# Kernel optimization log

Measured on AMD Instinct MI355X. Metric: run time of the kernel, lower is better.

Reference implementation:

```python
import jax, jax.numpy as jnp
import numpy as np

NUM_EXPERTS = 8
HIDDEN = 2048
FFN = 1376
CAPACITY_FACTOR = 1.25
SCORE_SCALE = 1.0


def setup_inputs() -> dict:
    key = jax.random.key(0)
    k = jax.random.split(key, 6)
    T = 8192
    x = jax.random.normal(k[0], (T, HIDDEN), dtype=jnp.float32)
    topK_indices = jax.random.randint(k[1], (T,), 0, NUM_EXPERTS, dtype=jnp.int64)
    topK_scores = jax.random.uniform(k[2], (T,), dtype=jnp.float32)
    s = 1.0 / np.sqrt(HIDDEN)
    w_gate = jax.random.normal(k[3], (NUM_EXPERTS, HIDDEN, FFN), dtype=jnp.float32) * s
    w_up = jax.random.normal(k[4], (NUM_EXPERTS, HIDDEN, FFN), dtype=jnp.float32) * s
    w_down = jax.random.normal(k[5], (NUM_EXPERTS, FFN, HIDDEN), dtype=jnp.float32) * (1.0 / np.sqrt(FFN))
    return {"x": x, "topK_indices": topK_indices, "topK_scores": topK_scores,
            "w_gate": w_gate, "w_up": w_up, "w_down": w_down}


def reference(x, topK_indices, topK_scores, w_gate, w_up, w_down):
    T, D = x.shape
    E = w_gate.shape[0]
    capacity = int(CAPACITY_FACTOR * T / E)  # static (depends only on shapes)
    # position of each token within its assigned expert (deterministic drop:
    # keep the first `capacity` tokens in sequence order per expert)
    oh = jax.nn.one_hot(topK_indices, E, dtype=jnp.int32)          # [T,E]
    rank = jnp.take_along_axis(jnp.cumsum(oh, axis=0) - 1,
                               topK_indices[:, None].astype(jnp.int32), axis=1)[:, 0]
    keep = rank < capacity                                          # [T]
    # dispatch into per-expert capacity buffers; dropped tokens go to dummy slot
    slot = jnp.where(keep, topK_indices.astype(jnp.int32) * capacity + rank, E * capacity)
    buf = jnp.zeros((E * capacity + 1, D), x.dtype)
    buf = buf.at[slot].set(jnp.where(keep[:, None], x, jnp.zeros_like(x)))
    xe = buf[:E * capacity].reshape(E, capacity, D)                 # [E,C,D]
    # per-expert SwiGLU MLP as grouped GEMMs
    h = jax.nn.silu(jnp.einsum('ecd,edf->ecf', xe, w_gate)) * jnp.einsum('ecd,edf->ecf', xe, w_up)
    out = jnp.einsum('ecf,efd->ecd', h, w_down).reshape(E * capacity, D)
    out = jnp.concatenate([out, jnp.zeros((1, D), out.dtype)], axis=0)
    # combine: dropped tokens -> zero (dropped_padding='zero'), gate-score fusion
    y = out[slot] * keep[:, None].astype(out.dtype)
    y = y * (topK_scores[:, None] * SCORE_SCALE)
    return y
```

## Files before the change

### kernel.cpp

```cpp
#include <hip/hip_runtime.h>
#include <hip/hip_bf16.h>
#include <cstdint>
#include <cstddef>

#define NTOK 8192
#define DH   2048
#define DF   1376
#define DFP  1408
#define NE   8
#define CAP  1280

typedef __bf16 bf16x8 __attribute__((ext_vector_type(8)));
typedef float  f32x4  __attribute__((ext_vector_type(4)));

#define BARRIER() asm volatile("s_barrier" ::: "memory")
#define WAITV(n)  asm volatile("s_waitcnt vmcnt(" #n ")" ::: "memory")
#define SETPRIO(n) __builtin_amdgcn_s_setprio(n)

__device__ __forceinline__ uint32_t pk2(float a, float b) {
  float2 f; f.x = a; f.y = b;
  union { __hip_bfloat162 h; uint32_t u; } cv;
  cv.h = __float22bfloat162_rn(f);
  return cv.u;
}
__device__ __forceinline__ ushort bf16bits(float a) {
  return (ushort)(pk2(a, 0.f) & 0xFFFFu);
}
__device__ __forceinline__ void gload16(const ushort* g, ushort* l) {
  __builtin_amdgcn_global_load_lds(
      (const __attribute__((address_space(1))) uint32_t*)(const void*)g,
      (__attribute__((address_space(3))) uint32_t*)(void*)l,
      16, 0, 0);
}

__device__ __forceinline__ void rp_src(int o, int& row, int& ko) {
  int p = o >> 7;
  int g = ((o >> 4) & 7) ^ (p & 7);
  row = p * 2 + (g >> 2);
  ko  = (g & 3) * 8;
}
__device__ __forceinline__ int rp_off(int row, int l4) {
  return ((row >> 1) << 7) + (((((row & 1) << 2) + l4) ^ ((row >> 1) & 7)) << 4);
}

__global__ void routing_kernel(const int* __restrict__ idx, int* __restrict__ tok_slot,
                               int* __restrict__ tok_keep) {
  __shared__ int cnt[256][NE];
  const int t = threadIdx.x;
  for (int s = t; s < NE * CAP; s += 256) tok_slot[s] = -1;
  unsigned long long cA = 0ull, cB = 0ull;
  const int per = NTOK / 256, base = t * per;
  for (int i = 0; i < per; ++i) {
    int e = idx[base + i];
    unsigned long long inc = 1ull << ((e & 3) * 16);
    if (e < 4) cA += inc; else cB += inc;
  }
#pragma unroll
  for (int e = 0; e < 4; ++e) cnt[t][e]     = (int)((cA >> (e * 16)) & 0xFFFF);
#pragma unroll
  for (int e = 0; e < 4; ++e) cnt[t][4 + e] = (int)((cB >> (e * 16)) & 0xFFFF);
  __syncthreads();
  if (t < NE) {
    int run = 0;
    for (int i = 0; i < 256; ++i) { int c = cnt[i][t]; cnt[i][t] = run; run += c; }
  }
  __syncthreads();
  cA = 0ull; cB = 0ull;
#pragma unroll
  for (int e = 0; e < 4; ++e) cA |= (unsigned long long)(cnt[t][e] & 0xFFFF) << (e * 16);
#pragma unroll
  for (int e = 0; e < 4; ++e) cB |= (unsigned long long)(cnt[t][4 + e] & 0xFFFF) << (e * 16);
  for (int i = 0; i < per; ++i) {
    int token = base + i;
    int e = idx[token];
    int sh = (e & 3) * 16;
    int r = (int)(((e < 4 ? cA : cB) >> sh) & 0xFFFF);
    unsigned long long inc = 1ull << sh;
    if (e < 4) cA += inc; else cB += inc;
    bool keep = (r < CAP);
    tok_keep[token] = keep ? 1 : 0;
    if (keep) tok_slot[e * CAP + r] = token;
  }
}

__global__ void zero_dropped(const int* __restrict__ keep, float* __restrict__ y) {
  if (keep[blockIdx.x]) return;
  float4 z = {0.f, 0.f, 0.f, 0.f};
  float* p = y + (size_t)blockIdx.x * DH + threadIdx.x * 8;
  *(float4*)p = z;
  *(float4*)(p + 4) = z;
}

__global__ void convert_x(const float* __restrict__ x, ushort* __restrict__ xb) {
  int i = (blockIdx.x * 256 + threadIdx.x) * 8;
  float4 a = *(const float4*)(x + i);
  float4 b = *(const float4*)(x + i + 4);
  uint4 p = { pk2(a.x, a.y), pk2(a.z, a.w), pk2(b.x, b.y), pk2(b.z, b.w) };
  *(uint4*)(xb + i) = p;
}

__global__ __launch_bounds__(256) void transpose_cvt(
    const float* __restrict__ in, ushort* __restrict__ out, int K, int N) {
  __shared__ ushort T[64][72];
  const int tid = threadIdx.x;
  const int n0 = blockIdx.x * 64, k0 = blockIdx.y * 64;
  const size_t eoff_in  = (size_t)blockIdx.z * K * N;
  const size_t eoff_out = (size_t)blockIdx.z * N * K;
  const int kr = tid >> 4;
  const int nc = (tid & 15) * 4;
#pragma unroll
  for (int it = 0; it < 4; ++it) {
    int k = k0 + kr + it * 16;
    int n = n0 + nc;
    float4 v = {0.f, 0.f, 0.f, 0.f};
    if (k < K && n + 4 <= N) v = *(const float4*)(in + eoff_in + (size_t)k * N + n);
    T[nc + 0][kr + it * 16] = bf16bits(v.x);
    T[nc + 1][kr + it * 16] = bf16bits(v.y);
    T[nc + 2][kr + it * 16] = bf16bits(v.z);
    T[nc + 3][kr + it * 16] = bf16bits(v.w);
  }
  __syncthreads();
  const int nr = tid >> 2;
  const int kc = tid & 3;
#pragma unroll
  for (int it = 0; it < 2; ++it) {
    int kloc = kc * 16 + it * 8;
    int n = n0 + nr, k = k0 + kloc;
    if (n < N && k + 8 <= K)
      *(uint4*)(out + eoff_out + (size_t)n * K + k) = *(const uint4*)&T[nr][kloc];
  }
}

__global__ void pad_h(ushort* __restrict__ h) {
  int idx = blockIdx.x * 512 + threadIdx.x;
  int row = idx >> 2, q = idx & 3;
  uint4 z = {0u, 0u, 0u, 0u};
  *(uint4*)(h + (size_t)row * DFP + DF + q * 8) = z;
}

__global__ __launch_bounds__(512, 1) void gemm_gateup3(
    const ushort* __restrict__ xb, const ushort* __restrict__ wgt,
    const ushort* __restrict__ wut, const int* __restrict__ tok_slot,
    ushort* __restrict__ h)
{
  __shared__ __align__(16) char sm[131072];
  const int tid = threadIdx.x, lane = tid & 63, wid = tid >> 6;
  const int wr = wid >> 1, wc = wid & 1;
  const int l15 = lane & 15, l4 = lane >> 4;

  int wgid = (blockIdx.x & 7) * 55 + (blockIdx.x >> 3);
  const int e = wgid / 55;
  const int rem = wgid - e * 55;
  const int mt = rem / 11, nt = rem - (rem / 11) * 11;
  const int n0 = nt * 128;

  const ushort* srcA[2]; const ushort* srcBg; const ushort* srcBu;
#pragma unroll
  for (int c = 0; c < 2; ++c) {
    int o = c * 8192 + wid * 1024 + lane * 16;
    int row, ko; rp_src(o, row, ko);
    int tk = tok_slot[e * CAP + mt * 256 + row];
    if (tk < 0) tk = 0;
    srcA[c] = xb + (size_t)tk * DH + ko;
  }
  {
    int o = wid * 1024 + lane * 16;
    int row, ko; rp_src(o, row, ko);
    int n = n0 + row; if (n > DF - 1) n = DF - 1;
    srcBg = wgt + ((size_t)e * DF + n) * DH + ko;
    srcBu = wut + ((size_t)e * DF + n) * DH + ko;
  }
  int aoff[4], boff[4];
#pragma unroll
  for (int i = 0; i < 4; ++i) aoff[i] = rp_off(wr * 64 + i * 16 + l15, l4);
#pragma unroll
  for (int j = 0; j < 4; ++j) boff[j] = rp_off(wc * 64 + j * 16 + l15, l4);
  const int dstw = wid * 1024;

  f32x4 accG[4][4], accU[4][4];
#pragma unroll
  for (int i = 0; i < 4; ++i)
#pragma unroll
    for (int j = 0; j < 4; ++j) {
      accG[i][j] = (f32x4){0.f, 0.f, 0.f, 0.f};
      accU[i][j] = (f32x4){0.f, 0.f, 0.f, 0.f};
    }

  const int NT = DH / 32;
#pragma unroll
  for (int t0 = 0; t0 < 3; ++t0) {
    int kk = t0 * 32;
    gload16(srcA[0] + kk, (ushort*)(sm + t0 * 16384 + dstw));
    gload16(srcA[1] + kk, (ushort*)(sm + t0 * 16384 + 8192 + dstw));
    gload16(srcBg   + kk, (ushort*)(sm + 65536 + t0 * 8192 + dstw));
    gload16(srcBu   + kk, (ushort*)(sm + 98304 + t0 * 8192 + dstw));
  }
  WAITV(8);
  BARRIER();

  for (int t = 0; t < NT; ++t) {
    const int r = t & 3, w = (t + 3) & 3;
    char* Ab  = sm + r * 16384;
    char* Bgb = sm + 65536 + r * 8192;
    char* Bub = sm + 98304 + r * 8192;
    bf16x8 a[4], bg[4], bu[4];
#pragma unroll
    for (int i = 0; i < 4; ++i) a[i]  = *(const bf16x8*)(Ab + aoff[i]);
#pragma unroll
    for (int j = 0; j < 4; ++j) bg[j] = *(const bf16x8*)(Bgb + boff[j]);
#pragma unroll
    for (int j = 0; j < 4; ++j) bu[j] = *(const bf16x8*)(Bub + boff[j]);
    if (t + 3 < NT) {
      int kk = (t + 3) * 32;
      gload16(srcA[0] + kk, (ushort*)(sm + w * 16384 + dstw));
      gload16(srcA[1] + kk, (ushort*)(sm + w * 16384 + 8192 + dstw));
      gload16(srcBg   + kk, (ushort*)(sm + 65536 + w * 8192 + dstw));
      gload16(srcBu   + kk, (ushort*)(sm + 98304 + w * 8192 + dstw));
    }
    SETPRIO(1);
#pragma unroll
    for (int j = 0; j < 4; ++j)
#pragma unroll
      for (int i = 0; i < 4; ++i)
        accG[i][j] = __builtin_amdgcn_mfma_f32_16x16x32_bf16(a[i], bg[j], accG[i][j], 0, 0, 0);
#pragma unroll
    for (int j = 0; j < 4; ++j)
#pragma unroll
      for (int i = 0; i < 4; ++i)
        accU[i][j] = __builtin_amdgcn_mfma_f32_16x16x32_bf16(a[i], bu[j], accU[i][j], 0, 0, 0);
    SETPRIO(0);
    if (t + 3 < NT)      { WAITV(8); }
    else if (t + 2 < NT) { WAITV(4); }
    else if (t + 1 < NT) { WAITV(0); }
    BARRIER();
  }
  const size_t rowbase = (size_t)(e * CAP + mt * 256 + wr * 64);
#pragma unroll
  for (int j = 0; j < 4; ++j) {
    int col = n0 + wc * 64 + j * 16 + l15;
    if (col < DF) {
#pragma unroll
      for (int i = 0; i < 4; ++i)
#pragma unroll
        for (int r2 = 0; r2 < 4; ++r2) {
          size_t row = rowbase + i * 16 + l4 * 4 + r2;
          float gv = accG[i][j][r2], uv = accU[i][j][r2];
          h[row * DFP + col] = bf16bits(gv / (1.f + __expf(-gv)) * uv);
        }
    }
  }
}

__global__ __launch_bounds__(512, 1) void gemm_down3(
    const ushort* __restrict__ h, const ushort* __restrict__ wdt,
    const int* __restrict__ tok_slot, const float* __restrict__ scores,
    float* __restrict__ y)
{
  __shared__ __align__(16) char sm[100352];
  int* tokc = (int*)(sm + 98304);
  float* scc = (float*)(sm + 99328);
  const int tid = threadIdx.x, lane = tid & 63, wid = tid >> 6;
  const int wr = wid >> 1, wc = wid & 1;
  const int l15 = lane & 15, l4 = lane >> 4;

  int wgid = (blockIdx.x & 7) * 80 + (blockIdx.x >> 3);
  const int e = wgid / 80;
  const int rem = wgid - e * 80;
  const int mt = rem / 16, nt = rem & 15;
  const int n0 = nt * 128;

  if (tid < 256) {
    int tk = tok_slot[e * CAP + mt * 256 + tid];
    tokc[tid] = tk;
    scc[tid] = (tk >= 0) ? scores[tk] : 0.f;
  }
  __syncthreads();

  const size_t hrow0 = (size_t)(e * CAP + mt * 256);
  const ushort* srcA[2]; const ushort* srcB;
#pragma unroll
  for (int c = 0; c < 2; ++c) {
    int o = c * 8192 + wid * 1024 + lane * 16;
    int row, ko; rp_src(o, row, ko);
    srcA[c] = h + (hrow0 + row) * DFP + ko;
  }
  {
    int o = wid * 1024 + lane * 16;
    int row, ko; rp_src(o, row, ko);
    srcB = wdt + ((size_t)e * DH + n0 + row) * DF + ko;
  }
  int aoff[4], boff[4];
#pragma unroll
  for (int i = 0; i < 4; ++i) aoff[i] = rp_off(wr * 64 + i * 16 + l15, l4);
#pragma unroll
  for (int j = 0; j < 4; ++j) boff[j] = rp_off(wc * 64 + j * 16 + l15, l4);
  const int dstw = wid * 1024;

  f32x4 acc[4][4];
#pragma unroll
  for (int i = 0; i < 4; ++i)
#pragma unroll
    for (int j = 0; j < 4; ++j) acc[i][j] = (f32x4){0.f, 0.f, 0.f, 0.f};

  const int NT = DFP / 32;
#pragma unroll
  for (int t0 = 0; t0 < 3; ++t0) {
    int kk = t0 * 32;
    gload16(srcA[0] + kk, (ushort*)(sm + t0 * 16384 + dstw));
    gload16(srcA[1] + kk, (ushort*)(sm + t0 * 16384 + 8192 + dstw));
    gload16(srcB    + kk, (ushort*)(sm + 65536 + t0 * 8192 + dstw));
  }
  WAITV(6);
  BARRIER();

  for (int t = 0; t < NT; ++t) {
    const int r = t & 3, w = (t + 3) & 3;
    char* Ab = sm + r * 16384;
    char* Bb = sm + 65536 + r * 8192;
    bf16x8 a[4], b[4];
#pragma unroll
    for (int i = 0; i < 4; ++i) a[i] = *(const bf16x8*)(Ab + aoff[i]);
#pragma unroll
    for (int j = 0; j < 4; ++j) b[j] = *(const bf16x8*)(Bb + boff[j]);
    if (t + 3 < NT) {
      int kk = (t + 3) * 32;
      gload16(srcA[0] + kk, (ushort*)(sm + w * 16384 + dstw));
      gload16(srcA[1] + kk, (ushort*)(sm + w * 16384 + 8192 + dstw));
      gload16(srcB    + kk, (ushort*)(sm + 65536 + w * 8192 + dstw));
    }
    SETPRIO(1);
#pragma unroll
    for (int j = 0; j < 4; ++j)
#pragma unroll
      for (int i = 0; i < 4; ++i)
        acc[i][j] = __builtin_amdgcn_mfma_f32_16x16x32_bf16(a[i], b[j], acc[i][j], 0, 0, 0);
    SETPRIO(0);
    if (t + 3 < NT)      { WAITV(6); }
    else if (t + 2 < NT) { WAITV(3); }
    else if (t + 1 < NT) { WAITV(0); }
    BARRIER();
  }
  int tkr[4][4]; float sr[4][4];
#pragma unroll
  for (int i = 0; i < 4; ++i)
#pragma unroll
    for (int r = 0; r < 4; ++r) {
      int rl = wr * 64 + i * 16 + l4 * 4 + r;
      tkr[i][r] = tokc[rl];
      sr[i][r]  = scc[rl];
    }
#pragma unroll
  for (int j = 0; j < 4; ++j) {
    int col = n0 + wc * 64 + j * 16 + l15;
#pragma unroll
    for (int i = 0; i < 4; ++i)
#pragma unroll
      for (int r = 0; r < 4; ++r)
        if (tkr[i][r] >= 0)
          y[(size_t)tkr[i][r] * DH + col] = acc[i][j][r] * sr[i][r];
  }
}

extern "C" void kernel_launch(void* const* d_in, const int* in_sizes, int n_in,
                              void* d_out, int out_size, void* d_ws, size_t ws_size,
                              hipStream_t stream) {
  const float* x   = (const float*)d_in[0];
  const int*   idx = (const int*)d_in[1];
  const float* sc  = (const float*)d_in[2];
  const float* wg  = (const float*)d_in[3];
  const float* wu  = (const float*)d_in[4];
  const float* wd  = (const float*)d_in[5];
  float* y = (float*)d_out;

  const size_t OFF_KEEP = 40960;
  const size_t OFF_H    = 73728;
  const size_t SZ_H     = (size_t)NE * CAP * DFP * 2;
  const size_t OFF_XB   = OFF_H + SZ_H;
  const size_t SZ_XB    = (size_t)NTOK * DH * 2;
  const size_t OFF_WGT  = OFF_XB + SZ_XB;
  const size_t SZ_W     = (size_t)NE * DH * DF * 2;
  const size_t OFF_WUT  = OFF_WGT + SZ_W;

  int* tok_slot = (int*)d_ws;
  int* tok_keep = (int*)((char*)d_ws + OFF_KEEP);
  ushort* hbuf = (ushort*)((char*)d_ws + OFF_H);
  ushort* xb   = (ushort*)((char*)d_ws + OFF_XB);
  ushort* wgt  = (ushort*)((char*)d_ws + OFF_WGT);
  ushort* wut  = (ushort*)((char*)d_ws + OFF_WUT);
  ushort* wdt  = wgt;

  hipLaunchKernelGGL(routing_kernel, dim3(1), dim3(256), 0, stream, idx, tok_slot, tok_keep);
  hipLaunchKernelGGL(zero_dropped, dim3(NTOK), dim3(256), 0, stream, tok_keep, y);
  hipLaunchKernelGGL(convert_x, dim3(NTOK * DH / 2048), dim3(256), 0, stream, x, xb);
  hipLaunchKernelGGL(transpose_cvt, dim3((DF + 63) / 64, DH / 64, NE), dim3(256), 0, stream,
                     wg, wgt, DH, DF);
  hipLaunchKernelGGL(transpose_cvt, dim3((DF + 63) / 64, DH / 64, NE), dim3(256), 0, stream,
                     wu, wut, DH, DF);
  hipLaunchKernelGGL(pad_h, dim3(80), dim3(512), 0, stream, hbuf);
  hipLaunchKernelGGL(gemm_gateup3, dim3(440), dim3(512), 0, stream,
                     xb, wgt, wut, tok_slot, hbuf);
  hipLaunchKernelGGL(transpose_cvt, dim3(DH / 64, (DF + 63) / 64, NE), dim3(256), 0, stream,
                     wd, wdt, DF, DH);
  hipLaunchKernelGGL(gemm_down3, dim3(640), dim3(512), 0, stream,
                     hbuf, wdt, tok_slot, sc, y);
}
```

Measured before the change: 356.0 us.

## Split GEMM main loops into two barrier-separated phases interleaving loads and MFMAs

Both grouped-GEMM kernels now split each K-step into two halves. Each half issues part of the LDS reads and global-to-LDS prefetches, then runs a barrier, an lgkmcnt wait and a scheduling barrier around half of the MFMA work. The aim is a ping-pong style schedule where memory issue from some waves overlaps matrix math in others, with tighter control over compiler instruction ordering. The cost is extra barriers per iteration, which may add stalls if the waves do not actually stagger.

```diff
diff --git a/kernel.cpp b/kernel.cpp
--- a/kernel.cpp
+++ b/kernel.cpp
@@ -15,6 +15,8 @@
 
 #define BARRIER() asm volatile("s_barrier" ::: "memory")
 #define WAITV(n)  asm volatile("s_waitcnt vmcnt(" #n ")" ::: "memory")
+#define LGKM0()   asm volatile("s_waitcnt lgkmcnt(0)" ::: "memory")
+#define SCHED0()  __builtin_amdgcn_sched_barrier(0)
 #define SETPRIO(n) __builtin_amdgcn_s_setprio(n)
 
 __device__ __forceinline__ uint32_t pk2(float a, float b) {
@@ -203,35 +205,44 @@
     char* Ab  = sm + r * 16384;
     char* Bgb = sm + 65536 + r * 8192;
     char* Bub = sm + 98304 + r * 8192;
+    const int kk = (t + 3) * 32;
     bf16x8 a[4], bg[4], bu[4];
 #pragma unroll
     for (int i = 0; i < 4; ++i) a[i]  = *(const bf16x8*)(Ab + aoff[i]);
 #pragma unroll
     for (int j = 0; j < 4; ++j) bg[j] = *(const bf16x8*)(Bgb + boff[j]);
+    if (t + 3 < NT) {
+      gload16(srcA[0] + kk, (ushort*)(sm + w * 16384 + dstw));
+      gload16(srcA[1] + kk, (ushort*)(sm + w * 16384 + 8192 + dstw));
+    }
+    BARRIER();
+    LGKM0(); SCHED0();
+    SETPRIO(1);
+#pragma unroll
+    for (int j = 0; j < 4; ++j)
+#pragma unroll
+      for (int i = 0; i < 4; ++i)
+        accG[i][j] = __builtin_amdgcn_mfma_f32_16x16x32_bf16(a[i], bg[j], accG[i][j], 0, 0, 0);
+    SETPRIO(0); SCHED0();
+    BARRIER();
 #pragma unroll
     for (int j = 0; j < 4; ++j) bu[j] = *(const bf16x8*)(Bub + boff[j]);
     if (t + 3 < NT) {
-      int kk = (t + 3) * 32;
-      gload16(srcA[0] + kk, (ushort*)(sm + w * 16384 + dstw));
-      gload16(srcA[1] + kk, (ushort*)(sm + w * 16384 + 8192 + dstw));
-      gload16(srcBg   + kk, (ushort*)(sm + 65536 + w * 8192 + dstw));
-      gload16(srcBu   + kk, (ushort*)(sm + 98304 + w * 8192 + dstw));
-    }
-    SETPRIO(1);
-#pragma unroll
-    for (int j = 0; j < 4; ++j)
-#pragma unroll
-      for (int i = 0; i < 4; ++i)
-        accG[i][j] = __builtin_amdgcn_mfma_f32_16x16x32_bf16(a[i], bg[j], accG[i][j], 0, 0, 0);
-#pragma unroll
-    for (int j = 0; j < 4; ++j)
-#pragma unroll
-      for (int i = 0; i < 4; ++i)
-        accU[i][j] = __builtin_amdgcn_mfma_f32_16x16x32_bf16(a[i], bu[j], accU[i][j], 0, 0, 0);
-    SETPRIO(0);
+      gload16(srcBg + kk, (ushort*)(sm + 65536 + w * 8192 + dstw));
+      gload16(srcBu + kk, (ushort*)(sm + 98304 + w * 8192 + dstw));
+    }
     if (t + 3 < NT)      { WAITV(8); }
     else if (t + 2 < NT) { WAITV(4); }
     else if (t + 1 < NT) { WAITV(0); }
+    BARRIER();
+    LGKM0(); SCHED0();
+    SETPRIO(1);
+#pragma unroll
+    for (int j = 0; j < 4; ++j)
+#pragma unroll
+      for (int i = 0; i < 4; ++i)
+        accU[i][j] = __builtin_amdgcn_mfma_f32_16x16x32_bf16(a[i], bu[j], accU[i][j], 0, 0, 0);
+    SETPRIO(0); SCHED0();
     BARRIER();
   }
   const size_t rowbase = (size_t)(e * CAP + mt * 256 + wr * 64);
@@ -317,27 +328,42 @@
     const int r = t & 3, w = (t + 3) & 3;
     char* Ab = sm + r * 16384;
     char* Bb = sm + 65536 + r * 8192;
+    const int kk = (t + 3) * 32;
     bf16x8 a[4], b[4];
 #pragma unroll
     for (int i = 0; i < 4; ++i) a[i] = *(const bf16x8*)(Ab + aoff[i]);
-#pragma unroll
-    for (int j = 0; j < 4; ++j) b[j] = *(const bf16x8*)(Bb + boff[j]);
+    b[0] = *(const bf16x8*)(Bb + boff[0]);
+    b[1] = *(const bf16x8*)(Bb + boff[1]);
     if (t + 3 < NT) {
-      int kk = (t + 3) * 32;
       gload16(srcA[0] + kk, (ushort*)(sm + w * 16384 + dstw));
       gload16(srcA[1] + kk, (ushort*)(sm + w * 16384 + 8192 + dstw));
-      gload16(srcB    + kk, (ushort*)(sm + 65536 + w * 8192 + dstw));
-    }
+    }
+    BARRIER();
+    LGKM0(); SCHED0();
     SETPRIO(1);
 #pragma unroll
-    for (int j = 0; j < 4; ++j)
-#pragma unroll
-      for (int i = 0; i < 4; ++i)
-        acc[i][j] = __builtin_amdgcn_mfma_f32_16x16x32_bf16(a[i], b[j], acc[i][j], 0, 0, 0);
-    SETPRIO(0);
+    for (int i = 0; i < 4; ++i) {
+      acc[i][0] = __builtin_amdgcn_mfma_f32_16x16x32_bf16(a[i], b[0], acc[i][0], 0, 0, 0);
+      acc[i][1] = __builtin_amdgcn_mfma_f32_16x16x32_bf16(a[i], b[1], acc[i][1], 0, 0, 0);
+    }
+    SETPRIO(0); SCHED0();
+    BARRIER();
+    b[2] = *(const bf16x8*)(Bb + boff[2]);
+    b[3] = *(const bf16x8*)(Bb + boff[3]);
+    if (t + 3 < NT)
+      gload16(srcB + kk, (ushort*)(sm + 65536 + w * 8192 + dstw));
     if (t + 3 < NT)      { WAITV(6); }
     else if (t + 2 < NT) { WAITV(3); }
     else if (t + 1 < NT) { WAITV(0); }
+    BARRIER();
+    LGKM0(); SCHED0();
+    SETPRIO(1);
+#pragma unroll
+    for (int i = 0; i < 4; ++i) {
+      acc[i][2] = __builtin_amdgcn_mfma_f32_16x16x32_bf16(a[i], b[2], acc[i][2], 0, 0, 0);
+      acc[i][3] = __builtin_amdgcn_mfma_f32_16x16x32_bf16(a[i], b[3], acc[i][3], 0, 0, 0);
+    }
+    SETPRIO(0); SCHED0();
     BARRIER();
   }
   int tkr[4][4]; float sr[4][4];
```

New measurement: 349.3 us. Within noise of the previous version (-1.9%).

## Restructure MoE GEMM pipelines with 64-wide K stages and larger down tiles

Applied to the files above, without the earlier changes.

The gate/up GEMM moves from a 4-stage 32-wide K ring to two 64-wide K stages, each split into half-steps. Gate and up MFMAs are interleaved with staggered global-to-LDS loads, explicit LDS waits and scheduling barriers. The down GEMM grows to a 256x256 output tile per block with 8x4 accumulators per wave and halves the grid, and its weights are stored with a padded K stride. The x conversion and the zeroing of dropped rows are fused into one kernel. These changes aim to increase data reuse, overlap loads with MFMA and cut launch overhead, at the cost of more barriers, higher register pressure and reliance on padded weight columns being finite.

```diff
diff --git a/kernel.cpp b/kernel.cpp
--- a/kernel.cpp
+++ b/kernel.cpp
@@ -15,6 +15,8 @@
 
 #define BARRIER() asm volatile("s_barrier" ::: "memory")
 #define WAITV(n)  asm volatile("s_waitcnt vmcnt(" #n ")" ::: "memory")
+#define LGKM0()   asm volatile("s_waitcnt lgkmcnt(0)" ::: "memory")
+#define SCHED0()  __builtin_amdgcn_sched_barrier(0)
 #define SETPRIO(n) __builtin_amdgcn_s_setprio(n)
 
 __device__ __forceinline__ uint32_t pk2(float a, float b) {
@@ -83,29 +85,29 @@
   }
 }
 
-__global__ void zero_dropped(const int* __restrict__ keep, float* __restrict__ y) {
-  if (keep[blockIdx.x]) return;
-  float4 z = {0.f, 0.f, 0.f, 0.f};
-  float* p = y + (size_t)blockIdx.x * DH + threadIdx.x * 8;
-  *(float4*)p = z;
-  *(float4*)(p + 4) = z;
-}
-
-__global__ void convert_x(const float* __restrict__ x, ushort* __restrict__ xb) {
-  int i = (blockIdx.x * 256 + threadIdx.x) * 8;
-  float4 a = *(const float4*)(x + i);
-  float4 b = *(const float4*)(x + i + 4);
+__global__ void xconv_zero(const float* __restrict__ x, const int* __restrict__ keep,
+                           ushort* __restrict__ xb, float* __restrict__ y) {
+  const int row = blockIdx.x;
+  const int c = threadIdx.x * 8;
+  const size_t off = (size_t)row * DH + c;
+  float4 a = *(const float4*)(x + off);
+  float4 b = *(const float4*)(x + off + 4);
   uint4 p = { pk2(a.x, a.y), pk2(a.z, a.w), pk2(b.x, b.y), pk2(b.z, b.w) };
-  *(uint4*)(xb + i) = p;
+  *(uint4*)(xb + off) = p;
+  if (!keep[row]) {
+    float4 z = {0.f, 0.f, 0.f, 0.f};
+    *(float4*)(y + off) = z;
+    *(float4*)(y + off + 4) = z;
+  }
 }
 
 __global__ __launch_bounds__(256) void transpose_cvt(
-    const float* __restrict__ in, ushort* __restrict__ out, int K, int N) {
+    const float* __restrict__ in, ushort* __restrict__ out, int K, int N, int ostride) {
   __shared__ ushort T[64][72];
   const int tid = threadIdx.x;
   const int n0 = blockIdx.x * 64, k0 = blockIdx.y * 64;
   const size_t eoff_in  = (size_t)blockIdx.z * K * N;
-  const size_t eoff_out = (size_t)blockIdx.z * N * K;
+  const size_t eoff_out = (size_t)blockIdx.z * N * ostride;
   const int kr = tid >> 4;
   const int nc = (tid & 15) * 4;
 #pragma unroll
@@ -127,7 +129,7 @@
     int kloc = kc * 16 + it * 8;
     int n = n0 + nr, k = k0 + kloc;
     if (n < N && k + 8 <= K)
-      *(uint4*)(out + eoff_out + (size_t)n * K + k) = *(const uint4*)&T[nr][kloc];
+      *(uint4*)(out + eoff_out + (size_t)n * ostride + k) = *(const uint4*)&T[nr][kloc];
   }
 }
 
@@ -138,7 +140,7 @@
   *(uint4*)(h + (size_t)row * DFP + DF + q * 8) = z;
 }
 
-__global__ __launch_bounds__(512, 1) void gemm_gateup3(
+__global__ __launch_bounds__(512, 2) void gemm_gateup5(
     const ushort* __restrict__ xb, const ushort* __restrict__ wgt,
     const ushort* __restrict__ wut, const int* __restrict__ tok_slot,
     ushort* __restrict__ h)
@@ -151,20 +153,20 @@
   int wgid = (blockIdx.x & 7) * 55 + (blockIdx.x >> 3);
   const int e = wgid / 55;
   const int rem = wgid - e * 55;
-  const int mt = rem / 11, nt = rem - (rem / 11) * 11;
+  const int mt = rem % 5, nt = rem / 5;
   const int n0 = nt * 128;
 
   const ushort* srcA[2]; const ushort* srcBg; const ushort* srcBu;
 #pragma unroll
   for (int c = 0; c < 2; ++c) {
-    int o = c * 8192 + wid * 1024 + lane * 16;
+    int o = c * 8192 + tid * 16;
     int row, ko; rp_src(o, row, ko);
     int tk = tok_slot[e * CAP + mt * 256 + row];
     if (tk < 0) tk = 0;
     srcA[c] = xb + (size_t)tk * DH + ko;
   }
   {
-    int o = wid * 1024 + lane * 16;
+    int o = tid * 16;
     int row, ko; rp_src(o, row, ko);
     int n = n0 + row; if (n > DF - 1) n = DF - 1;
     srcBg = wgt + ((size_t)e * DF + n) * DH + ko;
@@ -177,6 +179,15 @@
   for (int j = 0; j < 4; ++j) boff[j] = rp_off(wc * 64 + j * 16 + l15, l4);
   const int dstw = wid * 1024;
 
+#define GU_A(s,kh)  (sm + (s) * 32768 + (kh) * 16384)
+#define GU_BG(s,kh) (sm + 65536 + (s) * 16384 + (kh) * 8192)
+#define GU_BU(s,kh) (sm + 98304 + (s) * 16384 + (kh) * 8192)
+#define GU_STA(s,kh,ko_) { \
+  gload16(srcA[0] + (ko_), (ushort*)(GU_A(s,kh) + dstw)); \
+  gload16(srcA[1] + (ko_), (ushort*)(GU_A(s,kh) + 8192 + dstw)); }
+#define GU_STBG(s,kh,ko_) gload16(srcBg + (ko_), (ushort*)(GU_BG(s,kh) + dstw))
+#define GU_STBU(s,kh,ko_) gload16(srcBu + (ko_), (ushort*)(GU_BU(s,kh) + dstw))
+
   f32x4 accG[4][4], accU[4][4];
 #pragma unroll
   for (int i = 0; i < 4; ++i)
@@ -186,52 +197,72 @@
       accU[i][j] = (f32x4){0.f, 0.f, 0.f, 0.f};
     }
 
-  const int NT = DH / 32;
-#pragma unroll
-  for (int t0 = 0; t0 < 3; ++t0) {
-    int kk = t0 * 32;
-    gload16(srcA[0] + kk, (ushort*)(sm + t0 * 16384 + dstw));
-    gload16(srcA[1] + kk, (ushort*)(sm + t0 * 16384 + 8192 + dstw));
-    gload16(srcBg   + kk, (ushort*)(sm + 65536 + t0 * 8192 + dstw));
-    gload16(srcBu   + kk, (ushort*)(sm + 98304 + t0 * 8192 + dstw));
-  }
-  WAITV(8);
+  const int NT = DH / 64;
+  GU_STA(0, 0, 0);  GU_STBG(0, 0, 0);  GU_STBU(0, 0, 0);
+  GU_STA(0, 1, 32); GU_STBG(0, 1, 32); GU_STBU(0, 1, 32);
+  GU_STA(1, 0, 64); GU_STBG(1, 0, 64); GU_STBU(1, 0, 64);
+  WAITV(9);
   BARRIER();
 
-  for (int t = 0; t < NT; ++t) {
-    const int r = t & 3, w = (t + 3) & 3;
-    char* Ab  = sm + r * 16384;
-    char* Bgb = sm + 65536 + r * 8192;
-    char* Bub = sm + 98304 + r * 8192;
-    bf16x8 a[4], bg[4], bu[4];
-#pragma unroll
-    for (int i = 0; i < 4; ++i) a[i]  = *(const bf16x8*)(Ab + aoff[i]);
-#pragma unroll
-    for (int j = 0; j < 4; ++j) bg[j] = *(const bf16x8*)(Bgb + boff[j]);
-#pragma unroll
-    for (int j = 0; j < 4; ++j) bu[j] = *(const bf16x8*)(Bub + boff[j]);
-    if (t + 3 < NT) {
-      int kk = (t + 3) * 32;
-      gload16(srcA[0] + kk, (ushort*)(sm + w * 16384 + dstw));
-      gload16(srcA[1] + kk, (ushort*)(sm + w * 16384 + 8192 + dstw));
-      gload16(srcBg   + kk, (ushort*)(sm + 65536 + w * 8192 + dstw));
-      gload16(srcBu   + kk, (ushort*)(sm + 98304 + w * 8192 + dstw));
-    }
-    SETPRIO(1);
-#pragma unroll
-    for (int j = 0; j < 4; ++j)
-#pragma unroll
-      for (int i = 0; i < 4; ++i)
-        accG[i][j] = __builtin_amdgcn_mfma_f32_16x16x32_bf16(a[i], bg[j], accG[i][j], 0, 0, 0);
-#pragma unroll
-    for (int j = 0; j < 4; ++j)
-#pragma unroll
-      for (int i = 0; i < 4; ++i)
-        accU[i][j] = __builtin_amdgcn_mfma_f32_16x16x32_bf16(a[i], bu[j], accU[i][j], 0, 0, 0);
-    SETPRIO(0);
-    if (t + 3 < NT)      { WAITV(8); }
-    else if (t + 2 < NT) { WAITV(4); }
-    else if (t + 1 < NT) { WAITV(0); }
+  bf16x8 a0[4], a1[4], bb[4];
+  for (int u = 0; u < NT; ++u) {
+    const int s = u & 1;
+    const int k1 = (u + 1) * 64 + 32, k2 = (u + 2) * 64;
+#pragma unroll
+    for (int i = 0; i < 4; ++i) a0[i] = *(const bf16x8*)(GU_A(s, 0) + aoff[i]);
+#pragma unroll
+    for (int j = 0; j < 4; ++j) bb[j] = *(const bf16x8*)(GU_BG(s, 0) + boff[j]);
+    if (u + 1 < NT) { GU_STA(s ^ 1, 1, k1); GU_STBG(s ^ 1, 1, k1); }
+    BARRIER(); LGKM0(); SCHED0();
+    SETPRIO(1);
+#pragma unroll
+    for (int j = 0; j < 4; ++j)
+#pragma unroll
+      for (int i = 0; i < 4; ++i)
+        accG[i][j] = __builtin_amdgcn_mfma_f32_16x16x32_bf16(a0[i], bb[j], accG[i][j], 0, 0, 0);
+    SETPRIO(0); SCHED0();
+    if (u + 2 < NT) { WAITV(11); } else { WAITV(0); }
+    BARRIER();
+#pragma unroll
+    for (int j = 0; j < 4; ++j) bb[j] = *(const bf16x8*)(GU_BU(s, 0) + boff[j]);
+    if (u + 1 < NT) GU_STBU(s ^ 1, 1, k1);
+    BARRIER(); LGKM0(); SCHED0();
+    SETPRIO(1);
+#pragma unroll
+    for (int j = 0; j < 4; ++j)
+#pragma unroll
+      for (int i = 0; i < 4; ++i)
+        accU[i][j] = __builtin_amdgcn_mfma_f32_16x16x32_bf16(a0[i], bb[j], accU[i][j], 0, 0, 0);
+    SETPRIO(0); SCHED0();
+    if (u + 2 < NT) { WAITV(9); } else { WAITV(0); }
+    BARRIER();
+#pragma unroll
+    for (int i = 0; i < 4; ++i) a1[i] = *(const bf16x8*)(GU_A(s, 1) + aoff[i]);
+#pragma unroll
+    for (int j = 0; j < 4; ++j) bb[j] = *(const bf16x8*)(GU_BG(s, 1) + boff[j]);
+    if (u + 2 < NT) { GU_STA(s, 0, k2); GU_STBG(s, 0, k2); }
+    BARRIER(); LGKM0(); SCHED0();
+    SETPRIO(1);
+#pragma unroll
+    for (int j = 0; j < 4; ++j)
+#pragma unroll
+      for (int i = 0; i < 4; ++i)
+        accG[i][j] = __builtin_amdgcn_mfma_f32_16x16x32_bf16(a1[i], bb[j], accG[i][j], 0, 0, 0);
+    SETPRIO(0); SCHED0();
+    if (u + 2 < NT) { WAITV(11); } else { WAITV(0); }
+    BARRIER();
+#pragma unroll
+    for (int j = 0; j < 4; ++j) bb[j] = *(const bf16x8*)(GU_BU(s, 1) + boff[j]);
+    if (u + 2 < NT) GU_STBU(s, 0, k2);
+    BARRIER(); LGKM0(); SCHED0();
+    SETPRIO(1);
+#pragma unroll
+    for (int j = 0; j < 4; ++j)
+#pragma unroll
+      for (int i = 0; i < 4; ++i)
+        accU[i][j] = __builtin_amdgcn_mfma_f32_16x16x32_bf16(a1[i], bb[j], accU[i][j], 0, 0, 0);
+    SETPRIO(0); SCHED0();
+    if (u + 2 < NT) { WAITV(9); } else { WAITV(0); }
     BARRIER();
   }
   const size_t rowbase = (size_t)(e * CAP + mt * 256 + wr * 64);
@@ -251,23 +282,23 @@
   }
 }
 
-__global__ __launch_bounds__(512, 1) void gemm_down3(
+__global__ __launch_bounds__(512, 2) void gemm_down5(
     const ushort* __restrict__ h, const ushort* __restrict__ wdt,
     const int* __restrict__ tok_slot, const float* __restrict__ scores,
     float* __restrict__ y)
 {
-  __shared__ __align__(16) char sm[100352];
-  int* tokc = (int*)(sm + 98304);
-  float* scc = (float*)(sm + 99328);
+  __shared__ __align__(16) char sm[131072];
+  __shared__ int tokc[256];
+  __shared__ float scc[256];
   const int tid = threadIdx.x, lane = tid & 63, wid = tid >> 6;
-  const int wr = wid >> 1, wc = wid & 1;
+  const int wr = wid >> 2, wc = wid & 3;
   const int l15 = lane & 15, l4 = lane >> 4;
 
-  int wgid = (blockIdx.x & 7) * 80 + (blockIdx.x >> 3);
-  const int e = wgid / 80;
-  const int rem = wgid - e * 80;
-  const int mt = rem / 16, nt = rem & 15;
-  const int n0 = nt * 128;
+  int wgid = (blockIdx.x & 7) * 40 + (blockIdx.x >> 3);
+  const int e = wgid / 40;
+  const int rem = wgid - e * 40;
+  const int mt = rem % 5, nt = rem / 5;
+  const int n0 = nt * 256;
 
   if (tid < 256) {
     int tk = tok_slot[e * CAP + mt * 256 + tid];
@@ -277,87 +308,117 @@
   __syncthreads();
 
   const size_t hrow0 = (size_t)(e * CAP + mt * 256);
-  const ushort* srcA[2]; const ushort* srcB;
+  const ushort* srcA[2]; const ushort* srcB[2];
 #pragma unroll
   for (int c = 0; c < 2; ++c) {
-    int o = c * 8192 + wid * 1024 + lane * 16;
+    int o = c * 8192 + tid * 16;
     int row, ko; rp_src(o, row, ko);
     srcA[c] = h + (hrow0 + row) * DFP + ko;
-  }
-  {
-    int o = wid * 1024 + lane * 16;
-    int row, ko; rp_src(o, row, ko);
-    srcB = wdt + ((size_t)e * DH + n0 + row) * DF + ko;
-  }
-  int aoff[4], boff[4];
-#pragma unroll
-  for (int i = 0; i < 4; ++i) aoff[i] = rp_off(wr * 64 + i * 16 + l15, l4);
+    srcB[c] = wdt + ((size_t)e * DH + n0 + row) * DFP + ko;
+  }
+  int aoffL[4], aoffH[4], boff[4];
+#pragma unroll
+  for (int i = 0; i < 4; ++i) {
+    aoffL[i] = rp_off(wr * 128 + i * 16 + l15, l4);
+    aoffH[i] = rp_off(wr * 128 + 64 + i * 16 + l15, l4);
+  }
 #pragma unroll
   for (int j = 0; j < 4; ++j) boff[j] = rp_off(wc * 64 + j * 16 + l15, l4);
   const int dstw = wid * 1024;
 
-  f32x4 acc[4][4];
-#pragma unroll
-  for (int i = 0; i < 4; ++i)
+#define DN_A(s,kh) (sm + (s) * 32768 + (kh) * 16384)
+#define DN_B(s,kh) (sm + 65536 + (s) * 32768 + (kh) * 16384)
+#define DN_STA(s,kh,ko_) { \
+  gload16(srcA[0] + (ko_), (ushort*)(DN_A(s,kh) + dstw)); \
+  gload16(srcA[1] + (ko_), (ushort*)(DN_A(s,kh) + 8192 + dstw)); }
+#define DN_STB(s,kh,ko_) { \
+  gload16(srcB[0] + (ko_), (ushort*)(DN_B(s,kh) + dstw)); \
+  gload16(srcB[1] + (ko_), (ushort*)(DN_B(s,kh) + 8192 + dstw)); }
+
+  f32x4 acc[8][4];
+#pragma unroll
+  for (int i = 0; i < 8; ++i)
 #pragma unroll
     for (int j = 0; j < 4; ++j) acc[i][j] = (f32x4){0.f, 0.f, 0.f, 0.f};
 
-  const int NT = DFP / 32;
-#pragma unroll
-  for (int t0 = 0; t0 < 3; ++t0) {
-    int kk = t0 * 32;
-    gload16(srcA[0] + kk, (ushort*)(sm + t0 * 16384 + dstw));
-    gload16(srcA[1] + kk, (ushort*)(sm + t0 * 16384 + 8192 + dstw));
-    gload16(srcB    + kk, (ushort*)(sm + 65536 + t0 * 8192 + dstw));
-  }
-  WAITV(6);
+  const int NT = DFP / 64;
+  DN_STA(0, 0, 0);  DN_STB(0, 0, 0);
+  DN_STA(0, 1, 32); DN_STB(0, 1, 32);
+  DN_STA(1, 0, 64); DN_STB(1, 0, 64);
+  WAITV(8);
   BARRIER();
 
-  for (int t = 0; t < NT; ++t) {
-    const int r = t & 3, w = (t + 3) & 3;
-    char* Ab = sm + r * 16384;
-    char* Bb = sm + 65536 + r * 8192;
-    bf16x8 a[4], b[4];
-#pragma unroll
-    for (int i = 0; i < 4; ++i) a[i] = *(const bf16x8*)(Ab + aoff[i]);
-#pragma unroll
-    for (int j = 0; j < 4; ++j) b[j] = *(const bf16x8*)(Bb + boff[j]);
-    if (t + 3 < NT) {
-      int kk = (t + 3) * 32;
-      gload16(srcA[0] + kk, (ushort*)(sm + w * 16384 + dstw));
-      gload16(srcA[1] + kk, (ushort*)(sm + w * 16384 + 8192 + dstw));
-      gload16(srcB    + kk, (ushort*)(sm + 65536 + w * 8192 + dstw));
-    }
-    SETPRIO(1);
-#pragma unroll
-    for (int j = 0; j < 4; ++j)
-#pragma unroll
-      for (int i = 0; i < 4; ++i)
-        acc[i][j] = __builtin_amdgcn_mfma_f32_16x16x32_bf16(a[i], b[j], acc[i][j], 0, 0, 0);
-    SETPRIO(0);
-    if (t + 3 < NT)      { WAITV(6); }
-    else if (t + 2 < NT) { WAITV(3); }
-    else if (t + 1 < NT) { WAITV(0); }
-    BARRIER();
-  }
-  int tkr[4][4]; float sr[4][4];
-#pragma unroll
-  for (int i = 0; i < 4; ++i)
-#pragma unroll
-    for (int r = 0; r < 4; ++r) {
-      int rl = wr * 64 + i * 16 + l4 * 4 + r;
-      tkr[i][r] = tokc[rl];
-      sr[i][r]  = scc[rl];
-    }
+  bf16x8 av[4], bv[4];
+  for (int u = 0; u < NT; ++u) {
+    const int s = u & 1;
+    const int k1 = (u + 1) * 64 + 32, k2 = (u + 2) * 64;
+#pragma unroll
+    for (int i = 0; i < 4; ++i) av[i] = *(const bf16x8*)(DN_A(s, 0) + aoffL[i]);
+#pragma unroll
+    for (int j = 0; j < 4; ++j) bv[j] = *(const bf16x8*)(DN_B(s, 0) + boff[j]);
+    if (u + 1 < NT) DN_STA(s ^ 1, 1, k1);
+    BARRIER(); LGKM0(); SCHED0();
+    SETPRIO(1);
+#pragma unroll
+    for (int j = 0; j < 4; ++j)
+#pragma unroll
+      for (int i = 0; i < 4; ++i)
+        acc[i][j] = __builtin_amdgcn_mfma_f32_16x16x32_bf16(av[i], bv[j], acc[i][j], 0, 0, 0);
+    SETPRIO(0); SCHED0();
+    BARRIER();
+#pragma unroll
+    for (int i = 0; i < 4; ++i) av[i] = *(const bf16x8*)(DN_A(s, 0) + aoffH[i]);
+    if (u + 1 < NT) DN_STB(s ^ 1, 1, k1);
+    BARRIER(); LGKM0(); SCHED0();
+    SETPRIO(1);
+#pragma unroll
+    for (int j = 0; j < 4; ++j)
+#pragma unroll
+      for (int i = 0; i < 4; ++i)
+        acc[4 + i][j] = __builtin_amdgcn_mfma_f32_16x16x32_bf16(av[i], bv[j], acc[4 + i][j], 0, 0, 0);
+    SETPRIO(0); SCHED0();
+    if (u + 2 < NT) { WAITV(8); } else { WAITV(0); }
+    BARRIER();
+#pragma unroll
+    for (int i = 0; i < 4; ++i) av[i] = *(const bf16x8*)(DN_A(s, 1) + aoffL[i]);
+#pragma unroll
+    for (int j = 0; j < 4; ++j) bv[j] = *(const bf16x8*)(DN_B(s, 1) + boff[j]);
+    if (u + 2 < NT) DN_STA(s, 0, k2);
+    BARRIER(); LGKM0(); SCHED0();
+    SETPRIO(1);
+#pragma unroll
+    for (int j = 0; j < 4; ++j)
+#pragma unroll
+      for (int i = 0; i < 4; ++i)
+        acc[i][j] = __builtin_amdgcn_mfma_f32_16x16x32_bf16(av[i], bv[j], acc[i][j], 0, 0, 0);
+    SETPRIO(0); SCHED0();
+    BARRIER();
+#pragma unroll
+    for (int i = 0; i < 4; ++i) av[i] = *(const bf16x8*)(DN_A(s, 1) + aoffH[i]);
+    if (u + 2 < NT) DN_STB(s, 0, k2);
+    BARRIER(); LGKM0(); SCHED0();
+    SETPRIO(1);
+#pragma unroll
+    for (int j = 0; j < 4; ++j)
+#pragma unroll
+      for (int i = 0; i < 4; ++i)
+        acc[4 + i][j] = __builtin_amdgcn_mfma_f32_16x16x32_bf16(av[i], bv[j], acc[4 + i][j], 0, 0, 0);
+    SETPRIO(0); SCHED0();
+    if (u + 2 < NT) { WAITV(8); } else { WAITV(0); }
+    BARRIER();
+  }
 #pragma unroll
   for (int j = 0; j < 4; ++j) {
     int col = n0 + wc * 64 + j * 16 + l15;
 #pragma unroll
-    for (int i = 0; i < 4; ++i)
-#pragma unroll
-      for (int r = 0; r < 4; ++r)
-        if (tkr[i][r] >= 0)
-          y[(size_t)tkr[i][r] * DH + col] = acc[i][j][r] * sr[i][r];
+    for (int i = 0; i < 8; ++i)
+#pragma unroll
+      for (int r = 0; r < 4; ++r) {
+        int rl = wr * 128 + i * 16 + l4 * 4 + r;
+        int tk = tokc[rl];
+        if (tk >= 0)
+          y[(size_t)tk * DH + col] = acc[i][j][r] * scc[rl];
+      }
   }
 }
 
@@ -390,17 +451,16 @@
   ushort* wdt  = wgt;
 
   hipLaunchKernelGGL(routing_kernel, dim3(1), dim3(256), 0, stream, idx, tok_slot, tok_keep);
-  hipLaunchKernelGGL(zero_dropped, dim3(NTOK), dim3(256), 0, stream, tok_keep, y);
-  hipLaunchKernelGGL(convert_x, dim3(NTOK * DH / 2048), dim3(256), 0, stream, x, xb);
+  hipLaunchKernelGGL(xconv_zero, dim3(NTOK), dim3(256), 0, stream, x, tok_keep, xb, y);
   hipLaunchKernelGGL(transpose_cvt, dim3((DF + 63) / 64, DH / 64, NE), dim3(256), 0, stream,
-                     wg, wgt, DH, DF);
+                     wg, wgt, DH, DF, DH);
   hipLaunchKernelGGL(transpose_cvt, dim3((DF + 63) / 64, DH / 64, NE), dim3(256), 0, stream,
-                     wu, wut, DH, DF);
+                     wu, wut, DH, DF, DH);
   hipLaunchKernelGGL(pad_h, dim3(80), dim3(512), 0, stream, hbuf);
-  hipLaunchKernelGGL(gemm_gateup3, dim3(440), dim3(512), 0, stream,
+  hipLaunchKernelGGL(gemm_gateup5, dim3(440), dim3(512), 0, stream,
                      xb, wgt, wut, tok_slot, hbuf);
   hipLaunchKernelGGL(transpose_cvt, dim3(DH / 64, (DF + 63) / 64, NE), dim3(256), 0, stream,
-                     wd, wdt, DF, DH);
-  hipLaunchKernelGGL(gemm_down3, dim3(640), dim3(512), 0, stream,
+                     wd, wdt, DF, DH, DFP);
+  hipLaunchKernelGGL(gemm_down5, dim3(320), dim3(512), 0, stream,
                      hbuf, wdt, tok_slot, sc, y);
 }
```

New measurement: 342.5 us. -3.8%, faster.
